# Optimization experiments

Measured on AMD Instinct MI355X. Metric: run time of the kernel, lower is better.

## Reference

```python
import jax, jax.numpy as jnp
import numpy as np
from jax import lax

B, D_MODEL, T = 4, 256, 8192
D_STATE, D_CONV = 16, 4
D_INNER = 2 * D_MODEL          # expand=2.0
DT_RANK = (D_MODEL + 15) // 16 # ceil(d_model/16) = 16
EPS = 1e-5


def setup_inputs() -> dict:
    key = jax.random.key(0)
    ks = jax.random.split(key, 12)
    s = lambda k, shape, scale=0.02: (jax.random.normal(k, shape, jnp.float32) * scale)
    x = jax.random.normal(ks[0], (B, D_MODEL, T), jnp.float32)
    ln_w = jnp.ones((D_MODEL,), jnp.float32)
    ln_b = jnp.zeros((D_MODEL,), jnp.float32)
    in_proj_w = s(ks[1], (2 * D_INNER, D_MODEL))
    conv_w = s(ks[2], (D_INNER, 1, D_CONV), 0.1)
    conv_b = jnp.zeros((D_INNER,), jnp.float32)
    x_proj_w = s(ks[3], (DT_RANK + 2 * D_STATE, D_INNER))
    dt_proj_w = s(ks[4], (D_INNER, DT_RANK), 0.1)
    # bias init so softplus(dt_bias) ~ small positive dt, like mamba_ssm
    dt_proj_b = jnp.log(jnp.expm1(jax.random.uniform(ks[5], (D_INNER,), jnp.float32, 0.001, 0.1)))
    # S4D-real init: A_log = log(1..d_state) broadcast over d_inner
    A_log = jnp.log(jnp.tile(jnp.arange(1, D_STATE + 1, dtype=jnp.float32), (D_INNER, 1)))
    D = jnp.ones((D_INNER,), jnp.float32)
    out_proj_w = s(ks[6], (D_MODEL, D_INNER))
    return {"x": x, "ln_w": ln_w, "ln_b": ln_b, "in_proj_w": in_proj_w,
            "conv_w": conv_w, "conv_b": conv_b, "x_proj_w": x_proj_w,
            "dt_proj_w": dt_proj_w, "dt_proj_b": dt_proj_b, "A_log": A_log,
            "D": D, "out_proj_w": out_proj_w}


def _mamba_block(x, ln_w, ln_b, in_proj_w, conv_w, conv_b, x_proj_w,
                 dt_proj_w, dt_proj_b, A_log, D, out_proj_w):
    # x: (B, C, T)
    residual = x
    xt = jnp.transpose(x, (0, 2, 1))  # (B, T, C)
    # channel layernorm
    mu = jnp.mean(xt, axis=-1, keepdims=True)
    var = jnp.var(xt, axis=-1, keepdims=True)
    xn = (xt - mu) * lax.rsqrt(var + EPS) * ln_w + ln_b
    # in_proj -> x, z
    xz = jnp.einsum('btc,ec->bte', xn, in_proj_w)  # (B,T,2*d_inner)
    x_in, z = jnp.split(xz, 2, axis=-1)
    # causal depthwise conv over time
    xc = jnp.transpose(x_in, (0, 2, 1))  # (B, d_inner, T)
    xc = lax.conv_general_dilated(xc, conv_w, window_strides=(1,),
                                  padding=[(D_CONV - 1, 0)],
                                  dimension_numbers=('NCH', 'OIH', 'NCH'),
                                  feature_group_count=D_INNER)
    xc = xc + conv_b[None, :, None]
    u = jax.nn.silu(jnp.transpose(xc, (0, 2, 1)))  # (B,T,d_inner)
    # x_proj -> dt, B, C
    dbl = jnp.einsum('btd,ed->bte', u, x_proj_w)
    dt, Bm, Cm = jnp.split(dbl, [DT_RANK, DT_RANK + D_STATE], axis=-1)
    delta = jax.nn.softplus(jnp.einsum('btr,dr->btd', dt, dt_proj_w) + dt_proj_b)  # (B,T,d_inner)
    A = -jnp.exp(A_log)  # (d_inner, d_state)
    deltaA = jnp.exp(jnp.einsum('btd,dn->btdn', delta, A))          # (B,T,d,n)
    deltaBu = jnp.einsum('btd,btn->btdn', delta * u, Bm)            # (B,T,d,n)
    # selective scan over time
    def step(h, inp):
        dA_t, dBu_t, C_t = inp
        h = dA_t * h + dBu_t                       # (B,d,n)
        y = jnp.einsum('bdn,bn->bd', h, C_t)
        return h, y
    h0 = jnp.zeros((x.shape[0], D_INNER, D_STATE), x.dtype)
    _, ys = lax.scan(step, h0, (jnp.moveaxis(deltaA, 1, 0),
                                jnp.moveaxis(deltaBu, 1, 0),
                                jnp.moveaxis(Cm, 1, 0)))
    y = jnp.moveaxis(ys, 0, 1) + u * D             # (B,T,d_inner)
    y = y * jax.nn.silu(z)
    out = jnp.einsum('btd,cd->btc', y, out_proj_w)  # (B,T,C)
    return jnp.transpose(out, (0, 2, 1)) + residual


def reference(x, ln_w, ln_b, in_proj_w, conv_w, conv_b, x_proj_w,
              dt_proj_w, dt_proj_b, A_log, D, out_proj_w):
    return _mamba_block(x, ln_w, ln_b, in_proj_w, conv_w, conv_b, x_proj_w,
                        dt_proj_w, dt_proj_b, A_log, D, out_proj_w)
```

## Files before the change

kernel.cpp:

```cpp
#include <hip/hip_runtime.h>

typedef unsigned short u16;
typedef unsigned int u32;
typedef __bf16 bfx8 __attribute__((ext_vector_type(8)));
typedef float f32x4 __attribute__((ext_vector_type(4)));

#define Tn 8192
#define Bn 4
#define MTOT 32768
#define CH 128
#define TC 64

#define OFF_W     0ul
#define OFF_AL2   917504ul
#define OFF_XN    (1ul<<20)
#define OFF_XIN   (17ul<<20)
#define OFF_Z     (49ul<<20)
#define OFF_U     (81ul<<20)
#define OFF_DBLDT (113ul<<20)
#define OFF_BCF   (115ul<<20)
#define OFF_DELTA (119ul<<20)
#define OFF_P     (151ul<<20)
#define OFF_CC    (167ul<<20)

__device__ __forceinline__ float b2f(u16 h){ return __uint_as_float(((u32)h)<<16); }
__device__ __forceinline__ u16 f2b(float f){
  u32 u = __float_as_uint(f);
  return (u16)((u + 0x7FFFu + ((u>>16)&1u)) >> 16);
}
__device__ __forceinline__ float aexp2(float x){ float r; asm("v_exp_f32 %0, %1" : "=v"(r) : "v"(x)); return r; }
__device__ __forceinline__ float arcp (float x){ float r; asm("v_rcp_f32 %0, %1" : "=v"(r) : "v"(x)); return r; }
__device__ __forceinline__ float alog2(float x){ float r; asm("v_log_f32 %0, %1" : "=v"(r) : "v"(x)); return r; }
__device__ __forceinline__ float fsilu(float a){ return a*arcp(1.f + aexp2(-a*1.44269504f)); }
__device__ __forceinline__ float fsoftplus(float v){
  float r = 0.69314718f*alog2(1.f + aexp2(v*1.44269504f));
  return (v > 20.f) ? v : r;
}
typedef const __attribute__((address_space(1))) void* gp1_t;
typedef __attribute__((address_space(3))) void* lp3_t;
__device__ __forceinline__ void gload_lds16(const void* g, void* l){
  __builtin_amdgcn_global_load_lds((gp1_t)g, (lp3_t)l, 16, 0, 0);
}

__global__ void wconv_k(const float* __restrict__ inw, const float* __restrict__ xpw,
                        const float* __restrict__ dtw, const float* __restrict__ opw,
                        const float* __restrict__ alog, u16* __restrict__ W, float* __restrict__ aL2)
{
  int i = blockIdx.x*256 + threadIdx.x;
  if (i < 262144) { W[i] = f2b(inw[i]); return; }
  if (i < 294912) { int j = i - 262144; int r = j >> 9, k = j & 511;
    float v = (r < 16) ? xpw[r*512 + k] : ((r < 32) ? 0.f : xpw[(r-16)*512 + k]);
    W[i] = f2b(v); return; }
  if (i < 311296) { int j = i - 294912; int d = j >> 5, k = j & 31;
    W[i] = f2b((k < 16) ? dtw[d*16 + k] : 0.f); return; }
  if (i < 442368) { W[i] = f2b(opw[i - 311296]); return; }
  if (i < 450560) { int j = i - 442368; aL2[j] = -__expf(alog[j]) * 1.44269504088896f; return; }
}

__global__ __launch_bounds__(256)
void ln_k(const float* __restrict__ x, const float* __restrict__ lnw,
          const float* __restrict__ lnb, u16* __restrict__ xn)
{
  const int t0 = blockIdx.x*64, b = blockIdx.y;
  const int tid = threadIdx.x, cg = tid>>6, tl = tid&63;
  __shared__ float ps[4][64], pq[4][64], mu[64], rs[64];
  float s = 0.f, q = 0.f;
  for (int ci = 0; ci < 64; ci++){
    int c = ci*4 + cg;
    float v = x[((size_t)(b*256 + c))*Tn + t0 + tl];
    s += v; q += v*v;
  }
  ps[cg][tl] = s; pq[cg][tl] = q;
  __syncthreads();
  if (tid < 64){
    float S = ps[0][tid]+ps[1][tid]+ps[2][tid]+ps[3][tid];
    float Q = pq[0][tid]+pq[1][tid]+pq[2][tid]+pq[3][tid];
    float m = S*(1.f/256.f);
    float var = Q*(1.f/256.f) - m*m;
    mu[tid] = m; rs[tid] = rsqrtf(var + 1e-5f);
  }
  __syncthreads();
  const float w = lnw[tid&255], bb = lnb[tid&255];
  for (int t = 0; t < 64; t++){
    float v = x[((size_t)(b*256 + tid))*Tn + t0 + t];
    xn[((size_t)(b*Tn) + t0 + t)*256 + tid] = f2b((v - mu[t])*rs[t]*w + bb);
  }
}

template<int BN, int EPI>
__global__ __launch_bounds__(256)
void gemm_k(const u16* __restrict__ A, int lda,
            const u16* __restrict__ Bw, int ldb,
            u16* __restrict__ O, u16* __restrict__ O2, float* __restrict__ Of, int ldo,
            const float* __restrict__ bias, int K)
{
  constexpr int NFR = BN/32;
  __shared__ __align__(16) u16 sA[128*32];
  __shared__ __align__(16) u16 sB[BN*32];
  const int tid = threadIdx.x;
  const int m0 = blockIdx.x*128, n0 = blockIdx.y*BN;
  const int lane = tid & 63, wid = tid >> 6;
  const int wr = wid >> 1, wc = wid & 1;
  const int lr = lane & 15, g = lane >> 4;
  const f32x4 fz = {0.f,0.f,0.f,0.f};
  f32x4 acc[4][NFR];
  #pragma unroll
  for (int m=0;m<4;m++)
    #pragma unroll
    for (int n=0;n<NFR;n++) acc[m][n] = fz;
  const int nk = K >> 5;
  for (int kt = 0; kt < nk; ++kt){
    __syncthreads();
    #pragma unroll
    for (int i=0;i<2;i++){ int ci = i*256 + tid;
      gload_lds16(A + (size_t)(m0+(ci>>2))*lda + kt*32 + (ci&3)*8, sA + ci*8); }
    #pragma unroll
    for (int i=0;i<BN/64;i++){ int ci = i*256 + tid;
      gload_lds16(Bw + (size_t)(n0+(ci>>2))*ldb + kt*32 + (ci&3)*8, sB + ci*8); }
    __syncthreads();
    bfx8 af[4], bf[NFR];
    #pragma unroll
    for (int m=0;m<4;m++) af[m] = *(const bfx8*)(sA + (wr*64 + m*16 + lr)*32 + g*8);
    #pragma unroll
    for (int n=0;n<NFR;n++) bf[n] = *(const bfx8*)(sB + (wc*(BN/2) + n*16 + lr)*32 + g*8);
    #pragma unroll
    for (int m=0;m<4;m++)
      #pragma unroll
      for (int n=0;n<NFR;n++)
        acc[m][n] = __builtin_amdgcn_mfma_f32_16x16x32_bf16(af[m], bf[n], acc[m][n], 0, 0, 0);
  }
  #pragma unroll
  for (int m=0;m<4;m++)
    #pragma unroll
    for (int n=0;n<NFR;n++)
      #pragma unroll
      for (int r=0;r<4;r++){
        int row = m0 + wr*64 + m*16 + g*4 + r;
        int col = n0 + wc*(BN/2) + n*16 + lr;
        float v = acc[m][n][r];
        if (EPI == 1){
          O[(size_t)row*ldo + col] = f2b(fsoftplus(v + bias[col]));
        } else if (EPI == 2){
          if (col < 512) O[(size_t)row*512 + col] = f2b(v);
          else           O2[(size_t)row*512 + (col-512)] = f2b(v);
        } else {
          if (col < 32) O[(size_t)row*32 + col] = f2b(v);
          else          Of[(size_t)row*32 + (col-32)] = v;
        }
      }
}

__global__ __launch_bounds__(256)
void gemmot_k(const u16* __restrict__ A, const u16* __restrict__ Bw,
              const float* __restrict__ x, float* __restrict__ out)
{
  __shared__ __align__(16) u16 sA[128*32];
  __shared__ __align__(16) u16 sB[128*32];
  __shared__ float st[64][129];
  const int tid = threadIdx.x;
  const int m0 = blockIdx.x*128, n0 = blockIdx.y*128;
  const int lane = tid & 63, wid = tid >> 6;
  const int wr = wid >> 1, wc = wid & 1;
  const int lr = lane & 15, g = lane >> 4;
  const f32x4 fz = {0.f,0.f,0.f,0.f};
  f32x4 acc[4][4];
  #pragma unroll
  for (int m=0;m<4;m++)
    #pragma unroll
    for (int n=0;n<4;n++) acc[m][n] = fz;
  for (int kt = 0; kt < 16; ++kt){
    __syncthreads();
    #pragma unroll
    for (int i=0;i<2;i++){ int ci = i*256 + tid;
      gload_lds16(A + (size_t)(m0+(ci>>2))*512 + kt*32 + (ci&3)*8, sA + ci*8); }
    #pragma unroll
    for (int i=0;i<2;i++){ int ci = i*256 + tid;
      gload_lds16(Bw + (size_t)(n0+(ci>>2))*512 + kt*32 + (ci&3)*8, sB + ci*8); }
    __syncthreads();
    bfx8 af[4], bf[4];
    #pragma unroll
    for (int m=0;m<4;m++) af[m] = *(const bfx8*)(sA + (wr*64 + m*16 + lr)*32 + g*8);
    #pragma unroll
    for (int n=0;n<4;n++) bf[n] = *(const bfx8*)(sB + (wc*64 + n*16 + lr)*32 + g*8);
    #pragma unroll
    for (int m=0;m<4;m++)
      #pragma unroll
      for (int n=0;n<4;n++)
        acc[m][n] = __builtin_amdgcn_mfma_f32_16x16x32_bf16(af[m], bf[n], acc[m][n], 0, 0, 0);
  }
  const int b = m0 >> 13, t0 = m0 & 8191;
  const int tl = tid & 63, cgrp = tid >> 6;
  for (int hf=0; hf<2; hf++){
    __syncthreads();
    if (wr == hf){
      #pragma unroll
      for (int m=0;m<4;m++)
        #pragma unroll
        for (int n=0;n<4;n++)
          #pragma unroll
          for (int r=0;r<4;r++)
            st[m*16 + g*4 + r][wc*64 + n*16 + lr] = acc[m][n][r];
    }
    __syncthreads();
    const int tg = t0 + hf*64 + tl;
    #pragma unroll
    for (int ci=0; ci<32; ci++){
      int c = cgrp*32 + ci;
      size_t oa = ((size_t)(b*256) + n0 + c)*Tn + tg;
      out[oa] = st[tl][c] + x[oa];
    }
  }
}

__global__ __launch_bounds__(256)
void conv_k(const u16* __restrict__ xin, const float* __restrict__ cw,
            const float* __restrict__ cb, u16* __restrict__ u)
{
  const int t0 = blockIdx.x*32, d0 = blockIdx.y*64, b = blockIdx.z;
  const int tid = threadIdx.x;
  __shared__ float sx[35][64];
  __shared__ float sw[4][64];
  { int d = tid>>2, j = tid&3; sw[j][d] = cw[(d0+d)*4 + j]; }
  for (int i=0;i<9;i++){ int f = i*256 + tid; if (f < 35*64){
      int r = f>>6, dd = f&63; int t = t0 - 3 + r;
      sx[r][dd] = (t >= 0) ? b2f(xin[((size_t)(b*Tn)+t)*512 + d0+dd]) : 0.f; } }
  __syncthreads();
  const float cbv = cb[d0 + (tid&63)];
  for (int oi=0; oi<8; oi++){
    int f = oi*256 + tid; int tr = f>>6, dd = f&63;
    float a = cbv;
    #pragma unroll
    for (int j=0;j<4;j++) a += sw[j][dd]*sx[tr+j][dd];
    u[((size_t)(b*Tn)+t0+tr)*512 + d0+dd] = f2b(fsilu(a));
  }
}

__device__ __forceinline__ void powtree(float r1, float* e){
  float r2 = r1*r1;
  float r3 = r2*r1, r4 = r2*r2;
  float r5 = r4*r1, r6 = r4*r2, r7 = r4*r3, r8 = r4*r4;
  e[0]=r1; e[1]=r2; e[2]=r3; e[3]=r4; e[4]=r5; e[5]=r6; e[6]=r7; e[7]=r8;
  #pragma unroll
  for (int k=0;k<8;k++) e[8+k] = r8*e[k];
}

__global__ __launch_bounds__(256)
void scanA_k(const u16* __restrict__ delta, const u16* __restrict__ u,
             const float* __restrict__ bcf, const float* __restrict__ aL2,
             float* __restrict__ P, float* __restrict__ CC)
{
  const int ch = blockIdx.x, d = blockIdx.y*256 + threadIdx.x, b = blockIdx.z;
  const int t0 = ch*TC;
  float aL[16], h[16];
  #pragma unroll
  for (int i=0;i<4;i++) *(f32x4*)(aL+4*i) = *(const f32x4*)(aL2 + (size_t)d*16 + 4*i);
  #pragma unroll
  for (int n=0;n<16;n++) h[n] = 0.f;
  bool st = true;
  #pragma unroll
  for (int n=1;n<16;n++) st = st && (fabsf(aL[n] - (n+1)*aL[0]) <= 2e-4f*fabsf(aL[n]));
  const u16* dp = delta + (size_t)(b*Tn + t0)*512 + d;
  const u16* up = u     + (size_t)(b*Tn + t0)*512 + d;
  const float* bp = bcf + (size_t)(b*Tn + t0)*32;
  float sdlt = 0.f;
  const float aL0 = aL[0];
  if (st){
    #pragma unroll 4
    for (int t=0;t<TC;t++){
      float dlt = b2f(dp[(size_t)t*512]);
      float uu  = b2f(up[(size_t)t*512]);
      float Bv[16];
      #pragma unroll
      for (int i=0;i<4;i++) *(f32x4*)(Bv+4*i) = *(const f32x4*)(bp + (size_t)t*32 + 4*i);
      float du = dlt*uu; sdlt += dlt;
      float e[16];
      powtree(aexp2(dlt*aL0), e);
      #pragma unroll
      for (int n=0;n<16;n++)
        h[n] = fmaf(e[n], h[n], du*Bv[n]);
    }
  } else {
    #pragma unroll 2
    for (int t=0;t<TC;t++){
      float dlt = b2f(dp[(size_t)t*512]);
      float uu  = b2f(up[(size_t)t*512]);
      float Bv[16];
      #pragma unroll
      for (int i=0;i<4;i++) *(f32x4*)(Bv+4*i) = *(const f32x4*)(bp + (size_t)t*32 + 4*i);
      float du = dlt*uu; sdlt += dlt;
      #pragma unroll
      for (int n=0;n<16;n++)
        h[n] = fmaf(aexp2(dlt*aL[n]), h[n], du*Bv[n]);
    }
  }
  float Pq[16];
  #pragma unroll
  for (int n=0;n<16;n++) Pq[n] = aexp2(sdlt*aL[n]);
  size_t o = ((size_t)((b*CH+ch)*512 + d))<<4;
  #pragma unroll
  for (int i=0;i<4;i++){
    *(f32x4*)(P +o+4*i) = *(f32x4*)(Pq+4*i);
    *(f32x4*)(CC+o+4*i) = *(f32x4*)(h +4*i);
  }
}

__global__ __launch_bounds__(256)
void scanB_k(float* __restrict__ P, const float* __restrict__ CC)
{
  const int gid = blockIdx.x*256 + threadIdx.x;
  const int b = gid >> 13, r = gid & 8191;
  const size_t base = (size_t)b*CH*8192 + r;
  float h = 0.f;
  #pragma unroll 4
  for (int ch=0; ch<CH; ch++){
    size_t idx = base + (size_t)ch*8192;
    float Pv = P[idx];
    float cv = CC[idx];
    P[idx] = h;
    h = fmaf(Pv, h, cv);
  }
}

__global__ __launch_bounds__(256)
void scanC_k(const u16* __restrict__ delta, const u16* __restrict__ u,
             const float* __restrict__ bcf, const u16* __restrict__ z,
             const float* __restrict__ aL2, const float* __restrict__ h0,
             const float* __restrict__ Dp, u16* __restrict__ yg)
{
  const int ch = blockIdx.x, d = blockIdx.y*256 + threadIdx.x, b = blockIdx.z;
  const int t0 = ch*TC;
  float aL[16], h[16];
  #pragma unroll
  for (int i=0;i<4;i++) *(f32x4*)(aL+4*i) = *(const f32x4*)(aL2 + (size_t)d*16 + 4*i);
  size_t o = ((size_t)((b*CH+ch)*512 + d))<<4;
  #pragma unroll
  for (int i=0;i<4;i++) *(f32x4*)(h+4*i) = *(const f32x4*)(h0+o+4*i);
  bool st = true;
  #pragma unroll
  for (int n=1;n<16;n++) st = st && (fabsf(aL[n] - (n+1)*aL[0]) <= 2e-4f*fabsf(aL[n]));
  const float Dd = Dp[d];
  const float aL0 = aL[0];
  const u16* dp = delta + (size_t)(b*Tn + t0)*512 + d;
  const u16* up = u     + (size_t)(b*Tn + t0)*512 + d;
  const u16* zp = z     + (size_t)(b*Tn + t0)*512 + d;
  const float* bp = bcf + (size_t)(b*Tn + t0)*32;
  u16* yp = yg + (size_t)(b*Tn + t0)*512 + d;
  if (st){
    #pragma unroll 2
    for (int t=0;t<TC;t++){
      float dlt = b2f(dp[(size_t)t*512]);
      float uu  = b2f(up[(size_t)t*512]);
      float zz  = b2f(zp[(size_t)t*512]);
      float Bv[16], Cv[16];
      #pragma unroll
      for (int i=0;i<4;i++){
        *(f32x4*)(Bv+4*i) = *(const f32x4*)(bp + (size_t)t*32 + 4*i);
        *(f32x4*)(Cv+4*i) = *(const f32x4*)(bp + (size_t)t*32 + 16 + 4*i);
      }
      float du = dlt*uu;
      float e[16];
      powtree(aexp2(dlt*aL0), e);
      float p0=0.f, p1=0.f, p2=0.f, p3=0.f;
      #pragma unroll
      for (int n=0;n<16;n+=4){
        h[n]   = fmaf(e[n],   h[n],   du*Bv[n]);   p0 = fmaf(h[n],   Cv[n],   p0);
        h[n+1] = fmaf(e[n+1], h[n+1], du*Bv[n+1]); p1 = fmaf(h[n+1], Cv[n+1], p1);
        h[n+2] = fmaf(e[n+2], h[n+2], du*Bv[n+2]); p2 = fmaf(h[n+2], Cv[n+2], p2);
        h[n+3] = fmaf(e[n+3], h[n+3], du*Bv[n+3]); p3 = fmaf(h[n+3], Cv[n+3], p3);
      }
      float p = (p0+p1) + (p2+p3);
      float gy = (p + uu*Dd) * fsilu(zz);
      yp[(size_t)t*512] = f2b(gy);
    }
  } else {
    #pragma unroll 2
    for (int t=0;t<TC;t++){
      float dlt = b2f(dp[(size_t)t*512]);
      float uu  = b2f(up[(size_t)t*512]);
      float zz  = b2f(zp[(size_t)t*512]);
      float Bv[16], Cv[16];
      #pragma unroll
      for (int i=0;i<4;i++){
        *(f32x4*)(Bv+4*i) = *(const f32x4*)(bp + (size_t)t*32 + 4*i);
        *(f32x4*)(Cv+4*i) = *(const f32x4*)(bp + (size_t)t*32 + 16 + 4*i);
      }
      float du = dlt*uu;
      float p0 = 0.f;
      #pragma unroll
      for (int n=0;n<16;n++){
        h[n] = fmaf(aexp2(dlt*aL[n]), h[n], du*Bv[n]);
        p0 = fmaf(h[n], Cv[n], p0);
      }
      float gy = (p0 + uu*Dd) * fsilu(zz);
      yp[(size_t)t*512] = f2b(gy);
    }
  }
}

extern "C" void kernel_launch(void* const* d_in, const int* in_sizes, int n_in,
                              void* d_out, int out_size, void* d_ws, size_t ws_size,
                              hipStream_t stream)
{
  const float* x    = (const float*)d_in[0];
  const float* lnw  = (const float*)d_in[1];
  const float* lnb  = (const float*)d_in[2];
  const float* inw  = (const float*)d_in[3];
  const float* cw   = (const float*)d_in[4];
  const float* cb   = (const float*)d_in[5];
  const float* xpw  = (const float*)d_in[6];
  const float* dtw  = (const float*)d_in[7];
  const float* dtb  = (const float*)d_in[8];
  const float* alog = (const float*)d_in[9];
  const float* Dp   = (const float*)d_in[10];
  const float* opw  = (const float*)d_in[11];
  float* out = (float*)d_out;
  char* ws = (char*)d_ws;

  u16*   W     = (u16*)(ws + OFF_W);
  float* aL2   = (float*)(ws + OFF_AL2);
  u16*   xn    = (u16*)(ws + OFF_XN);
  u16*   xin   = (u16*)(ws + OFF_XIN);
  u16*   z     = (u16*)(ws + OFF_Z);
  u16*   u     = (u16*)(ws + OFF_U);
  u16*   dblDT = (u16*)(ws + OFF_DBLDT);
  float* bcf   = (float*)(ws + OFF_BCF);
  u16*   delta = (u16*)(ws + OFF_DELTA);
  float* P     = (float*)(ws + OFF_P);
  float* CC    = (float*)(ws + OFF_CC);
  u16*   yg    = xin;

  wconv_k<<<1760, 256, 0, stream>>>(inw, xpw, dtw, opw, alog, W, aL2);
  ln_k<<<dim3(Tn/64, Bn), 256, 0, stream>>>(x, lnw, lnb, xn);
  gemm_k<128,2><<<dim3(MTOT/128, 8), 256, 0, stream>>>(xn, 256, W, 256, xin, z, nullptr, 512, nullptr, 256);
  conv_k<<<dim3(Tn/32, 8, Bn), 256, 0, stream>>>(xin, cw, cb, u);
  gemm_k<64,3><<<dim3(MTOT/128, 1), 256, 0, stream>>>(u, 512, W + 262144, 512, dblDT, nullptr, bcf, 0, nullptr, 512);
  gemm_k<128,1><<<dim3(MTOT/128, 4), 256, 0, stream>>>(dblDT, 32, W + 294912, 32, delta, nullptr, nullptr, 512, dtb, 32);
  scanA_k<<<dim3(CH, 2, Bn), 256, 0, stream>>>(delta, u, bcf, aL2, P, CC);
  scanB_k<<<128, 256, 0, stream>>>(P, CC);
  scanC_k<<<dim3(CH, 2, Bn), 256, 0, stream>>>(delta, u, bcf, z, aL2, P, Dp, yg);
  gemmot_k<<<dim3(MTOT/128, 2), 256, 0, stream>>>(yg, W + 311296, x, out);
}
```

Before: 224.0 us.

## Split scan state dimension across two half-waves per channel

The chunked scan kernels now give each d_inner channel two lanes, each holding 8 of the 16 state entries. The partial C·h dot products are combined with a cross-half shuffle, and the grid is doubled. The powtree fast path, which derived all decay factors from one exp2 when A follows the S4D pattern, is removed, so every state element now computes its own exp2. This doubles thread-level parallelism and halves per-thread registers and serial work. In exchange, delta/u/z loads are duplicated across the two halves, exp2 work rises for the S4D-structured A, and half the lanes sit idle on the y store.

```diff
diff --git a/kernel.cpp b/kernel.cpp
--- a/kernel.cpp
+++ b/kernel.cpp
@@ -235,73 +235,45 @@
   }
 }
 
-__device__ __forceinline__ void powtree(float r1, float* e){
-  float r2 = r1*r1;
-  float r3 = r2*r1, r4 = r2*r2;
-  float r5 = r4*r1, r6 = r4*r2, r7 = r4*r3, r8 = r4*r4;
-  e[0]=r1; e[1]=r2; e[2]=r3; e[3]=r4; e[4]=r5; e[5]=r6; e[6]=r7; e[7]=r8;
-  #pragma unroll
-  for (int k=0;k<8;k++) e[8+k] = r8*e[k];
-}
-
 __global__ __launch_bounds__(256)
 void scanA_k(const u16* __restrict__ delta, const u16* __restrict__ u,
              const float* __restrict__ bcf, const float* __restrict__ aL2,
              float* __restrict__ P, float* __restrict__ CC)
 {
-  const int ch = blockIdx.x, d = blockIdx.y*256 + threadIdx.x, b = blockIdx.z;
+  const int ch = blockIdx.x, b = blockIdx.z;
+  const int tid = threadIdx.x, lane = tid & 63;
+  const int half = lane >> 5;
+  const int d = blockIdx.y*128 + (tid>>6)*32 + (lane & 31);
   const int t0 = ch*TC;
-  float aL[16], h[16];
-  #pragma unroll
-  for (int i=0;i<4;i++) *(f32x4*)(aL+4*i) = *(const f32x4*)(aL2 + (size_t)d*16 + 4*i);
-  #pragma unroll
-  for (int n=0;n<16;n++) h[n] = 0.f;
-  bool st = true;
-  #pragma unroll
-  for (int n=1;n<16;n++) st = st && (fabsf(aL[n] - (n+1)*aL[0]) <= 2e-4f*fabsf(aL[n]));
+  float aL[8], h[8];
+  #pragma unroll
+  for (int i=0;i<2;i++) *(f32x4*)(aL+4*i) = *(const f32x4*)(aL2 + (size_t)d*16 + half*8 + 4*i);
+  #pragma unroll
+  for (int k=0;k<8;k++) h[k] = 0.f;
   const u16* dp = delta + (size_t)(b*Tn + t0)*512 + d;
   const u16* up = u     + (size_t)(b*Tn + t0)*512 + d;
-  const float* bp = bcf + (size_t)(b*Tn + t0)*32;
+  const float* bp = bcf + (size_t)(b*Tn + t0)*32 + half*8;
   float sdlt = 0.f;
-  const float aL0 = aL[0];
-  if (st){
-    #pragma unroll 4
-    for (int t=0;t<TC;t++){
-      float dlt = b2f(dp[(size_t)t*512]);
-      float uu  = b2f(up[(size_t)t*512]);
-      float Bv[16];
-      #pragma unroll
-      for (int i=0;i<4;i++) *(f32x4*)(Bv+4*i) = *(const f32x4*)(bp + (size_t)t*32 + 4*i);
-      float du = dlt*uu; sdlt += dlt;
-      float e[16];
-      powtree(aexp2(dlt*aL0), e);
-      #pragma unroll
-      for (int n=0;n<16;n++)
-        h[n] = fmaf(e[n], h[n], du*Bv[n]);
-    }
-  } else {
-    #pragma unroll 2
-    for (int t=0;t<TC;t++){
-      float dlt = b2f(dp[(size_t)t*512]);
-      float uu  = b2f(up[(size_t)t*512]);
-      float Bv[16];
-      #pragma unroll
-      for (int i=0;i<4;i++) *(f32x4*)(Bv+4*i) = *(const f32x4*)(bp + (size_t)t*32 + 4*i);
-      float du = dlt*uu; sdlt += dlt;
-      #pragma unroll
-      for (int n=0;n<16;n++)
-        h[n] = fmaf(aexp2(dlt*aL[n]), h[n], du*Bv[n]);
-    }
-  }
-  float Pq[16];
-  #pragma unroll
-  for (int n=0;n<16;n++) Pq[n] = aexp2(sdlt*aL[n]);
-  size_t o = ((size_t)((b*CH+ch)*512 + d))<<4;
-  #pragma unroll
-  for (int i=0;i<4;i++){
-    *(f32x4*)(P +o+4*i) = *(f32x4*)(Pq+4*i);
-    *(f32x4*)(CC+o+4*i) = *(f32x4*)(h +4*i);
-  }
+  #pragma unroll 4
+  for (int t=0;t<TC;t++){
+    float dlt = b2f(dp[(size_t)t*512]);
+    float uu  = b2f(up[(size_t)t*512]);
+    float Bv[8];
+    *(f32x4*)(Bv)   = *(const f32x4*)(bp + (size_t)t*32);
+    *(f32x4*)(Bv+4) = *(const f32x4*)(bp + (size_t)t*32 + 4);
+    float du = dlt*uu; sdlt += dlt;
+    #pragma unroll
+    for (int k=0;k<8;k++)
+      h[k] = fmaf(aexp2(dlt*aL[k]), h[k], du*Bv[k]);
+  }
+  float Pq[8];
+  #pragma unroll
+  for (int k=0;k<8;k++) Pq[k] = aexp2(sdlt*aL[k]);
+  size_t o = (((size_t)((b*CH+ch)*512 + d))<<4) + half*8;
+  *(f32x4*)(P +o)   = *(f32x4*)(Pq);
+  *(f32x4*)(P +o+4) = *(f32x4*)(Pq+4);
+  *(f32x4*)(CC+o)   = *(f32x4*)(h);
+  *(f32x4*)(CC+o+4) = *(f32x4*)(h+4);
 }
 
 __global__ __launch_bounds__(256)
@@ -327,73 +299,44 @@
              const float* __restrict__ aL2, const float* __restrict__ h0,
              const float* __restrict__ Dp, u16* __restrict__ yg)
 {
-  const int ch = blockIdx.x, d = blockIdx.y*256 + threadIdx.x, b = blockIdx.z;
+  const int ch = blockIdx.x, b = blockIdx.z;
+  const int tid = threadIdx.x, lane = tid & 63;
+  const int half = lane >> 5;
+  const int d = blockIdx.y*128 + (tid>>6)*32 + (lane & 31);
   const int t0 = ch*TC;
-  float aL[16], h[16];
-  #pragma unroll
-  for (int i=0;i<4;i++) *(f32x4*)(aL+4*i) = *(const f32x4*)(aL2 + (size_t)d*16 + 4*i);
-  size_t o = ((size_t)((b*CH+ch)*512 + d))<<4;
-  #pragma unroll
-  for (int i=0;i<4;i++) *(f32x4*)(h+4*i) = *(const f32x4*)(h0+o+4*i);
-  bool st = true;
-  #pragma unroll
-  for (int n=1;n<16;n++) st = st && (fabsf(aL[n] - (n+1)*aL[0]) <= 2e-4f*fabsf(aL[n]));
+  float aL[8], h[8];
+  #pragma unroll
+  for (int i=0;i<2;i++) *(f32x4*)(aL+4*i) = *(const f32x4*)(aL2 + (size_t)d*16 + half*8 + 4*i);
+  size_t o = (((size_t)((b*CH+ch)*512 + d))<<4) + half*8;
+  *(f32x4*)(h)   = *(const f32x4*)(h0+o);
+  *(f32x4*)(h+4) = *(const f32x4*)(h0+o+4);
   const float Dd = Dp[d];
-  const float aL0 = aL[0];
   const u16* dp = delta + (size_t)(b*Tn + t0)*512 + d;
   const u16* up = u     + (size_t)(b*Tn + t0)*512 + d;
   const u16* zp = z     + (size_t)(b*Tn + t0)*512 + d;
-  const float* bp = bcf + (size_t)(b*Tn + t0)*32;
+  const float* bp = bcf + (size_t)(b*Tn + t0)*32 + half*8;
   u16* yp = yg + (size_t)(b*Tn + t0)*512 + d;
-  if (st){
-    #pragma unroll 2
-    for (int t=0;t<TC;t++){
-      float dlt = b2f(dp[(size_t)t*512]);
-      float uu  = b2f(up[(size_t)t*512]);
-      float zz  = b2f(zp[(size_t)t*512]);
-      float Bv[16], Cv[16];
-      #pragma unroll
-      for (int i=0;i<4;i++){
-        *(f32x4*)(Bv+4*i) = *(const f32x4*)(bp + (size_t)t*32 + 4*i);
-        *(f32x4*)(Cv+4*i) = *(const f32x4*)(bp + (size_t)t*32 + 16 + 4*i);
-      }
-      float du = dlt*uu;
-      float e[16];
-      powtree(aexp2(dlt*aL0), e);
-      float p0=0.f, p1=0.f, p2=0.f, p3=0.f;
-      #pragma unroll
-      for (int n=0;n<16;n+=4){
-        h[n]   = fmaf(e[n],   h[n],   du*Bv[n]);   p0 = fmaf(h[n],   Cv[n],   p0);
-        h[n+1] = fmaf(e[n+1], h[n+1], du*Bv[n+1]); p1 = fmaf(h[n+1], Cv[n+1], p1);
-        h[n+2] = fmaf(e[n+2], h[n+2], du*Bv[n+2]); p2 = fmaf(h[n+2], Cv[n+2], p2);
-        h[n+3] = fmaf(e[n+3], h[n+3], du*Bv[n+3]); p3 = fmaf(h[n+3], Cv[n+3], p3);
-      }
-      float p = (p0+p1) + (p2+p3);
-      float gy = (p + uu*Dd) * fsilu(zz);
-      yp[(size_t)t*512] = f2b(gy);
+  #pragma unroll 2
+  for (int t=0;t<TC;t++){
+    float dlt = b2f(dp[(size_t)t*512]);
+    float uu  = b2f(up[(size_t)t*512]);
+    float zz  = b2f(zp[(size_t)t*512]);
+    float Bv[8], Cv[8];
+    *(f32x4*)(Bv)   = *(const f32x4*)(bp + (size_t)t*32);
+    *(f32x4*)(Bv+4) = *(const f32x4*)(bp + (size_t)t*32 + 4);
+    *(f32x4*)(Cv)   = *(const f32x4*)(bp + (size_t)t*32 + 16);
+    *(f32x4*)(Cv+4) = *(const f32x4*)(bp + (size_t)t*32 + 20);
+    float du = dlt*uu;
+    float p0=0.f, p1=0.f;
+    #pragma unroll
+    for (int k=0;k<8;k+=2){
+      h[k]   = fmaf(aexp2(dlt*aL[k]),   h[k],   du*Bv[k]);   p0 = fmaf(h[k],   Cv[k],   p0);
+      h[k+1] = fmaf(aexp2(dlt*aL[k+1]), h[k+1], du*Bv[k+1]); p1 = fmaf(h[k+1], Cv[k+1], p1);
     }
-  } else {
-    #pragma unroll 2
-    for (int t=0;t<TC;t++){
-      float dlt = b2f(dp[(size_t)t*512]);
-      float uu  = b2f(up[(size_t)t*512]);
-      float zz  = b2f(zp[(size_t)t*512]);
-      float Bv[16], Cv[16];
-      #pragma unroll
-      for (int i=0;i<4;i++){
-        *(f32x4*)(Bv+4*i) = *(const f32x4*)(bp + (size_t)t*32 + 4*i);
-        *(f32x4*)(Cv+4*i) = *(const f32x4*)(bp + (size_t)t*32 + 16 + 4*i);
-      }
-      float du = dlt*uu;
-      float p0 = 0.f;
-      #pragma unroll
-      for (int n=0;n<16;n++){
-        h[n] = fmaf(aexp2(dlt*aL[n]), h[n], du*Bv[n]);
-        p0 = fmaf(h[n], Cv[n], p0);
-      }
-      float gy = (p0 + uu*Dd) * fsilu(zz);
-      yp[(size_t)t*512] = f2b(gy);
-    }
+    float p = p0 + p1;
+    p += __shfl_xor(p, 32);
+    float gy = (p + uu*Dd) * fsilu(zz);
+    if (half == 0) yp[(size_t)t*512] = f2b(gy);
   }
 }
 
@@ -435,8 +378,8 @@
   conv_k<<<dim3(Tn/32, 8, Bn), 256, 0, stream>>>(xin, cw, cb, u);
   gemm_k<64,3><<<dim3(MTOT/128, 1), 256, 0, stream>>>(u, 512, W + 262144, 512, dblDT, nullptr, bcf, 0, nullptr, 512);
   gemm_k<128,1><<<dim3(MTOT/128, 4), 256, 0, stream>>>(dblDT, 32, W + 294912, 32, delta, nullptr, nullptr, 512, dtb, 32);
-  scanA_k<<<dim3(CH, 2, Bn), 256, 0, stream>>>(delta, u, bcf, aL2, P, CC);
+  scanA_k<<<dim3(CH, 4, Bn), 256, 0, stream>>>(delta, u, bcf, aL2, P, CC);
   scanB_k<<<128, 256, 0, stream>>>(P, CC);
-  scanC_k<<<dim3(CH, 2, Bn), 256, 0, stream>>>(delta, u, bcf, z, aL2, P, Dp, yg);
+  scanC_k<<<dim3(CH, 4, Bn), 256, 0, stream>>>(delta, u, bcf, z, aL2, P, Dp, yg);
   gemmot_k<<<dim3(MTOT/128, 2), 256, 0, stream>>>(yg, W + 311296, x, out);
 }
```

Result: slower. 282.2 us (+26.0%).
